# Kernel tuning notes

Measured on AMD Instinct MI355X. Metric: run time of the kernel, lower is better.

## Reference

```python
import jax, jax.numpy as jnp
import numpy as np

TAU = 1.0  # FLAGS.tau


def setup_inputs() -> dict:
    key = jax.random.key(0)
    k1, k2, k3, k4 = jax.random.split(key, 4)
    B, N, E, D_in, D_out = 64, 512, 8, 64, 64
    edge_features = jax.random.normal(k1, (B, N, N, E), dtype=jnp.float32)
    x = jax.random.normal(k2, (B * N, D_in), dtype=jnp.float32)
    # glorot init for weights, normal for coef (as in source)
    lim = np.sqrt(6.0 / (D_in + D_out))
    W = jax.random.uniform(k3, (D_in, D_out), dtype=jnp.float32, minval=-lim, maxval=lim)
    coef = jax.random.normal(k4, (E, 1), dtype=jnp.float32)
    return {"edge_features": edge_features, "x": x, "W": W, "coef": coef}


def reference(edge_features, x, W, coef):
    B, N, _, E = edge_features.shape
    D_out = W.shape[1]
    # node transform: [B*N, D_in] @ [D_in, D_out]
    pre_sup = (x @ W).reshape(B, N, D_out)
    # per-edge attention score: [B,N,N,E] @ [E,1] -> [B,N,N]
    scores = jnp.einsum('bije,e->bij', edge_features, coef[:, 0])
    adj = jax.nn.softmax(scores / TAU, axis=-1)
    # preprocess_adj: add self-loops, symmetric D^-1/2 (A+I) D^-1/2.
    # Block-diagonal structure means normalization is per-graph, so we stay batched
    # instead of materializing the [B*N, B*N] block-diagonal matrix.
    adj_hat = adj + jnp.eye(N, dtype=adj.dtype)
    d_inv_sqrt = jax.lax.rsqrt(adj_hat.sum(axis=-1))  # [B,N]
    adj_norm = adj_hat * d_inv_sqrt[:, :, None] * d_inv_sqrt[:, None, :]
    # adjacency-weighted aggregation (block-diagonal matmul == batched matmul)
    out = jnp.einsum('bij,bjd->bid', adj_norm, pre_sup).reshape(B * N, D_out)
    return jax.nn.relu(out)
```

## Files before the change

### kernel.cpp

```cpp
#include <hip/hip_runtime.h>
#include <hip/hip_bf16.h>
#include <math.h>

#define B_  64
#define N_  512
#define E_  8
#define D_  64
#define LDP 264

typedef float f32x4 __attribute__((ext_vector_type(4)));
typedef short s16x8 __attribute__((ext_vector_type(8)));
typedef unsigned short u16;
typedef unsigned int u32;

__device__ __forceinline__ u16 bf16_rne(float x) {
    u32 u = __float_as_uint(x);
    u = (u + 0x7fffu + ((u >> 16) & 1u)) >> 16;
    return (u16)u;
}

__device__ __forceinline__ float pair_sum(float x) {
    int y = __builtin_amdgcn_mov_dpp(__float_as_int(x), 0xB1, 0xF, 0xF, true);
    return x + __int_as_float(y);
}


__global__ __launch_bounds__(256) void presup_kernel(
    const float* __restrict__ x, const float* __restrict__ W,
    float* __restrict__ ps, u16* __restrict__ psT)
{
    __shared__ float Wl[64 * 64];
    const int t = threadIdx.x;
#pragma unroll
    for (int i = 0; i < 4; ++i)
        ((f32x4*)Wl)[t + i * 256] = ((const f32x4*)W)[t + i * 256];
    __syncthreads();

    const int d4  = (t & 15) * 4;
    const int r   = t >> 4;
    const int row = blockIdx.x * 16 + r;
    const float* xr = x + (size_t)row * 64;

    f32x4 acc = 0.f;
#pragma unroll
    for (int k = 0; k < 64; k += 4) {
        f32x4 xv = *(const f32x4*)&xr[k];
        f32x4 w0 = *(const f32x4*)&Wl[(k + 0) * 64 + d4];
        f32x4 w1 = *(const f32x4*)&Wl[(k + 1) * 64 + d4];
        f32x4 w2 = *(const f32x4*)&Wl[(k + 2) * 64 + d4];
        f32x4 w3 = *(const f32x4*)&Wl[(k + 3) * 64 + d4];
        acc += xv.x * w0;
        acc += xv.y * w1;
        acc += xv.z * w2;
        acc += xv.w * w3;
    }
    *(f32x4*)&ps[(size_t)row * 64 + d4] = acc;

    const int b  = row >> 9, rb = row & 511;
#pragma unroll
    for (int i = 0; i < 4; ++i)
        psT[((size_t)b * 64 + d4 + i) * 512 + rb] = bf16_rne(acc[i]);
}

__global__ __launch_bounds__(256, 2) void fused_kernel(
    const float* __restrict__ edge, const float* __restrict__ coef,
    const u16* __restrict__ psT, const float* __restrict__ ps,
    float* __restrict__ out)
{
    __shared__ u16  pl[4][16][LDP];
    __shared__ float dn[4][16];

    const int t = threadIdx.x, w = t >> 6, l = t & 63;
    const int b  = blockIdx.x >> 3;
    const int i0 = (blockIdx.x & 7) * 64 + w * 16;
    const int ln = l & 15, g = l >> 4;

    f32x4 cA, cB;
    cA.x = coef[0]; cA.y = coef[1]; cA.z = coef[2]; cA.w = coef[3];
    cB.x = coef[4]; cB.y = coef[5]; cB.z = coef[6]; cB.w = coef[7];
    const f32x4 ch = (l & 1) ? cB : cA;

    const float* ebase = edge + ((size_t)b * N_ + i0) * (size_t)(N_ * E_) + 4 * l;
    const u16*   Ab    = psT + ((size_t)b * 64 + ln) * 512 + g * 8;

    f32x4 acc0 = {0.f,0.f,0.f,0.f}, acc1 = acc0, acc2 = acc0, acc3 = acc0;

    auto LOADC = [&](f32x4 (&buf)[8], int c) {
        const float* rp = ebase + (size_t)(c & 15) * (N_ * E_) + (c >> 4) * 2048;
#pragma unroll
        for (int c2 = 0; c2 < 8; ++c2)
            buf[c2] = *(const f32x4*)(rp + c2 * 256);
    };

    auto COMPUTE = [&](const f32x4 (&buf)[8], int c) {
        const int r = c & 15;
        float ls = 0.f;
#pragma unroll
        for (int c2 = 0; c2 < 8; ++c2) {
            f32x4 e = buf[c2];
            float dd = e.x * ch.x + e.y * ch.y + e.z * ch.z + e.w * ch.w;
            dd = pair_sum(dd);
            float p = __expf(dd);
            ls += p;
            pl[w][r][c2 * 32 + (l >> 1)] = bf16_rne(p);
        }
#pragma unroll
        for (int off = 32; off; off >>= 1) ls += __shfl_xor(ls, off, 64);
        if (l == 0) dn[w][r] = (c >> 4) ? (dn[w][r] + ls) : ls;
    };

    auto MFMA = [&](int h) {
        s16x8 bf[8];
#pragma unroll
        for (int kk = 0; kk < 8; ++kk)
            bf[kk] = *(const s16x8*)&pl[w][ln][kk * 32 + g * 8];
#pragma unroll
        for (int kk = 0; kk < 8; ++kk) {
            const int ko = h * 256 + kk * 32;
            s16x8 a0 = *(const s16x8*)(Ab + (size_t)(0 * 16) * 512 + ko);
            s16x8 a1 = *(const s16x8*)(Ab + (size_t)(1 * 16) * 512 + ko);
            s16x8 a2 = *(const s16x8*)(Ab + (size_t)(2 * 16) * 512 + ko);
            s16x8 a3 = *(const s16x8*)(Ab + (size_t)(3 * 16) * 512 + ko);
            acc0 = __builtin_amdgcn_mfma_f32_16x16x32_bf16(a0, bf[kk], acc0, 0, 0, 0);
            acc1 = __builtin_amdgcn_mfma_f32_16x16x32_bf16(a1, bf[kk], acc1, 0, 0, 0);
            acc2 = __builtin_amdgcn_mfma_f32_16x16x32_bf16(a2, bf[kk], acc2, 0, 0, 0);
            acc3 = __builtin_amdgcn_mfma_f32_16x16x32_bf16(a3, bf[kk], acc3, 0, 0, 0);
        }
    };

    f32x4 bA[8], bB[8], bC[8], bD[8];
    LOADC(bA, 0); LOADC(bB, 1);
    for (int c = 0; c < 32; c += 4) {
        LOADC(bC, c + 2); LOADC(bD, c + 3);
        COMPUTE(bA, c);
        COMPUTE(bB, c + 1);
        if (c + 4 < 32) { LOADC(bA, c + 4); LOADC(bB, c + 5); }
        COMPUTE(bC, c + 2);
        COMPUTE(bD, c + 3);
        if ((c & 15) == 12) MFMA(c >> 4);
    }

    const float rs = 1.f / dn[w][ln];
    const int   i  = i0 + ln;
    const size_t rowoff = ((size_t)b * N_ + i) * 64;

#pragma unroll
    for (int mt = 0; mt < 4; ++mt) {
        f32x4 acc = (mt == 0) ? acc0 : (mt == 1) ? acc1 : (mt == 2) ? acc2 : acc3;
        const int d0 = mt * 16 + g * 4;
        f32x4 self = *(const f32x4*)&ps[rowoff + d0];
        f32x4 o;
#pragma unroll
        for (int cc = 0; cc < 4; ++cc)
            o[cc] = fmaxf(acc[cc] * rs + 0.5f * self[cc], 0.f);
        *(f32x4*)&out[rowoff + d0] = o;
    }
}

extern "C" void kernel_launch(void* const* d_in, const int* in_sizes, int n_in,
                              void* d_out, int out_size, void* d_ws, size_t ws_size,
                              hipStream_t stream) {
    const float* edge = (const float*)d_in[0];
    const float* x    = (const float*)d_in[1];
    const float* W    = (const float*)d_in[2];
    const float* coef = (const float*)d_in[3];
    float* out = (float*)d_out;

    char* ws = (char*)d_ws;
    float* ps  = (float*)ws;
    u16*   psT = (u16*)(ws + (8u << 20));

    presup_kernel<<<(B_ * N_) / 16, 256, 0, stream>>>(x, W, ps, psT);
    fused_kernel<<<B_ * 8, 256, 0, stream>>>(edge, coef, psT, ps, out);
}
```

Before: 130.0 us.

## Split each row tile's column range across two waves and reduce via LDS

Each block now covers 32 rows instead of 64, with pairs of waves each handling half of the 512 columns for 16 rows. The partial MFMA accumulators and softmax denominators are combined through shared memory after a barrier. This doubles the grid to 1024 blocks, halves the per-wave prefetch buffers, and raises the launch-bounds occupancy hint from 2 to 4, aiming to keep more loads of the edge tensor in flight. The cost is an extra LDS exchange, a block-wide sync, and idle waves during the epilogue.

```diff
diff --git a/kernel.cpp b/kernel.cpp
--- a/kernel.cpp
+++ b/kernel.cpp
@@ -62,7 +62,7 @@
         psT[((size_t)b * 64 + d4 + i) * 512 + rb] = bf16_rne(acc[i]);
 }
 
-__global__ __launch_bounds__(256, 2) void fused_kernel(
+__global__ __launch_bounds__(256, 4) void fused_kernel(
     const float* __restrict__ edge, const float* __restrict__ coef,
     const u16* __restrict__ psT, const float* __restrict__ ps,
     float* __restrict__ out)
@@ -71,8 +71,9 @@
     __shared__ float dn[4][16];
 
     const int t = threadIdx.x, w = t >> 6, l = t & 63;
-    const int b  = blockIdx.x >> 3;
-    const int i0 = (blockIdx.x & 7) * 64 + w * 16;
+    const int b  = blockIdx.x >> 4;
+    const int i0 = (blockIdx.x & 15) * 32 + (w >> 1) * 16;
+    const int h  = w & 1;
     const int ln = l & 15, g = l >> 4;
 
     f32x4 cA, cB;
@@ -80,20 +81,20 @@
     cB.x = coef[4]; cB.y = coef[5]; cB.z = coef[6]; cB.w = coef[7];
     const f32x4 ch = (l & 1) ? cB : cA;
 
-    const float* ebase = edge + ((size_t)b * N_ + i0) * (size_t)(N_ * E_) + 4 * l;
-    const u16*   Ab    = psT + ((size_t)b * 64 + ln) * 512 + g * 8;
+    const float* ebase = edge + ((size_t)b * N_ + i0) * (size_t)(N_ * E_)
+                              + h * 2048 + 4 * l;
+    const u16*   Ab    = psT + ((size_t)b * 64 + ln) * 512 + h * 256 + g * 8;
 
     f32x4 acc0 = {0.f,0.f,0.f,0.f}, acc1 = acc0, acc2 = acc0, acc3 = acc0;
 
-    auto LOADC = [&](f32x4 (&buf)[8], int c) {
-        const float* rp = ebase + (size_t)(c & 15) * (N_ * E_) + (c >> 4) * 2048;
+    auto LOADC = [&](f32x4 (&buf)[8], int r) {
+        const float* rp = ebase + (size_t)r * (N_ * E_);
 #pragma unroll
         for (int c2 = 0; c2 < 8; ++c2)
             buf[c2] = *(const f32x4*)(rp + c2 * 256);
     };
 
-    auto COMPUTE = [&](const f32x4 (&buf)[8], int c) {
-        const int r = c & 15;
+    auto COMPUTE = [&](const f32x4 (&buf)[8], int r) {
         float ls = 0.f;
 #pragma unroll
         for (int c2 = 0; c2 < 8; ++c2) {
@@ -106,54 +107,64 @@
         }
 #pragma unroll
         for (int off = 32; off; off >>= 1) ls += __shfl_xor(ls, off, 64);
-        if (l == 0) dn[w][r] = (c >> 4) ? (dn[w][r] + ls) : ls;
+        if (l == 0) dn[w][r] = ls;
     };
 
-    auto MFMA = [&](int h) {
-        s16x8 bf[8];
+    f32x4 bA[8], bB[8];
+    LOADC(bA, 0); LOADC(bB, 1);
 #pragma unroll
-        for (int kk = 0; kk < 8; ++kk)
-            bf[kk] = *(const s16x8*)&pl[w][ln][kk * 32 + g * 8];
-#pragma unroll
-        for (int kk = 0; kk < 8; ++kk) {
-            const int ko = h * 256 + kk * 32;
-            s16x8 a0 = *(const s16x8*)(Ab + (size_t)(0 * 16) * 512 + ko);
-            s16x8 a1 = *(const s16x8*)(Ab + (size_t)(1 * 16) * 512 + ko);
-            s16x8 a2 = *(const s16x8*)(Ab + (size_t)(2 * 16) * 512 + ko);
-            s16x8 a3 = *(const s16x8*)(Ab + (size_t)(3 * 16) * 512 + ko);
-            acc0 = __builtin_amdgcn_mfma_f32_16x16x32_bf16(a0, bf[kk], acc0, 0, 0, 0);
-            acc1 = __builtin_amdgcn_mfma_f32_16x16x32_bf16(a1, bf[kk], acc1, 0, 0, 0);
-            acc2 = __builtin_amdgcn_mfma_f32_16x16x32_bf16(a2, bf[kk], acc2, 0, 0, 0);
-            acc3 = __builtin_amdgcn_mfma_f32_16x16x32_bf16(a3, bf[kk], acc3, 0, 0, 0);
-        }
-    };
-
-    f32x4 bA[8], bB[8], bC[8], bD[8];
-    LOADC(bA, 0); LOADC(bB, 1);
-    for (int c = 0; c < 32; c += 4) {
-        LOADC(bC, c + 2); LOADC(bD, c + 3);
+    for (int c = 0; c < 16; c += 2) {
         COMPUTE(bA, c);
+        if (c + 2 < 16) LOADC(bA, c + 2);
         COMPUTE(bB, c + 1);
-        if (c + 4 < 32) { LOADC(bA, c + 4); LOADC(bB, c + 5); }
-        COMPUTE(bC, c + 2);
-        COMPUTE(bD, c + 3);
-        if ((c & 15) == 12) MFMA(c >> 4);
+        if (c + 3 < 16) LOADC(bB, c + 3);
     }
 
-    const float rs = 1.f / dn[w][ln];
-    const int   i  = i0 + ln;
-    const size_t rowoff = ((size_t)b * N_ + i) * 64;
+#pragma unroll
+    for (int kk = 0; kk < 8; ++kk) {
+        s16x8 bf = *(const s16x8*)&pl[w][ln][kk * 32 + g * 8];
+        const int ko = kk * 32;
+        s16x8 a0 = *(const s16x8*)(Ab + (size_t)(0 * 16) * 512 + ko);
+        s16x8 a1 = *(const s16x8*)(Ab + (size_t)(1 * 16) * 512 + ko);
+        s16x8 a2 = *(const s16x8*)(Ab + (size_t)(2 * 16) * 512 + ko);
+        s16x8 a3 = *(const s16x8*)(Ab + (size_t)(3 * 16) * 512 + ko);
+        acc0 = __builtin_amdgcn_mfma_f32_16x16x32_bf16(a0, bf, acc0, 0, 0, 0);
+        acc1 = __builtin_amdgcn_mfma_f32_16x16x32_bf16(a1, bf, acc1, 0, 0, 0);
+        acc2 = __builtin_amdgcn_mfma_f32_16x16x32_bf16(a2, bf, acc2, 0, 0, 0);
+        acc3 = __builtin_amdgcn_mfma_f32_16x16x32_bf16(a3, bf, acc3, 0, 0, 0);
+    }
+
+    if (h) {
+        float* ex = (float*)&pl[w][0][0];
+        *(f32x4*)&ex[(0 * 64 + l) * 4] = acc0;
+        *(f32x4*)&ex[(1 * 64 + l) * 4] = acc1;
+        *(f32x4*)&ex[(2 * 64 + l) * 4] = acc2;
+        *(f32x4*)&ex[(3 * 64 + l) * 4] = acc3;
+    }
+    __syncthreads();
+
+    if (!h) {
+        const float* ex = (const float*)&pl[w + 1][0][0];
+        acc0 += *(const f32x4*)&ex[(0 * 64 + l) * 4];
+        acc1 += *(const f32x4*)&ex[(1 * 64 + l) * 4];
+        acc2 += *(const f32x4*)&ex[(2 * 64 + l) * 4];
+        acc3 += *(const f32x4*)&ex[(3 * 64 + l) * 4];
+
+        const float rs = 1.f / (dn[w][ln] + dn[w + 1][ln]);
+        const int   i  = i0 + ln;
+        const size_t rowoff = ((size_t)b * N_ + i) * 64;
 
 #pragma unroll
-    for (int mt = 0; mt < 4; ++mt) {
-        f32x4 acc = (mt == 0) ? acc0 : (mt == 1) ? acc1 : (mt == 2) ? acc2 : acc3;
-        const int d0 = mt * 16 + g * 4;
-        f32x4 self = *(const f32x4*)&ps[rowoff + d0];
-        f32x4 o;
+        for (int mt = 0; mt < 4; ++mt) {
+            f32x4 acc = (mt == 0) ? acc0 : (mt == 1) ? acc1 : (mt == 2) ? acc2 : acc3;
+            const int d0 = mt * 16 + g * 4;
+            f32x4 self = *(const f32x4*)&ps[rowoff + d0];
+            f32x4 o;
 #pragma unroll
-        for (int cc = 0; cc < 4; ++cc)
-            o[cc] = fmaxf(acc[cc] * rs + 0.5f * self[cc], 0.f);
-        *(f32x4*)&out[rowoff + d0] = o;
+            for (int cc = 0; cc < 4; ++cc)
+                o[cc] = fmaxf(acc[cc] * rs + 0.5f * self[cc], 0.f);
+            *(f32x4*)&out[rowoff + d0] = o;
+        }
     }
 }
 
@@ -171,5 +182,5 @@
     u16*   psT = (u16*)(ws + (8u << 20));
 
     presup_kernel<<<(B_ * N_) / 16, 256, 0, stream>>>(x, W, ps, psT);
-    fused_kernel<<<B_ * 8, 256, 0, stream>>>(edge, coef, psT, ps, out);
+    fused_kernel<<<B_ * 16, 256, 0, stream>>>(edge, coef, psT, ps, out);
 }
```

Result: faster. 126.0 us (-3.1%).
